# Performance work log

Hardware: AMD Instinct MI355X
Metric: run time of the kernel (lower is better)

Reference implementation:

```python
import jax, jax.numpy as jnp
import numpy as np

NB, L, A, FEAT = 4, 256, 14, 128
MAX_AA, MAX_RELPOS = 22, 32
ATOM_N, ATOM_CA, ATOM_C = 0, 1, 2
INFEAT = 3 * FEAT + 26  # 26 = AngularEncoding.get_out_dim(2)
FREQ = jnp.array([1.0, 2.0, 3.0, 1.0, 0.5, 1.0 / 3.0], jnp.float32)


def _dihedral(p0, p1, p2, p3):
    v0 = p2 - p1
    v1 = p0 - p1
    v2 = p3 - p2
    u1 = jnp.cross(v0, v1)
    u2 = jnp.cross(v0, v2)
    n1 = u1 / jnp.linalg.norm(u1, axis=-1, keepdims=True)
    n2 = u2 / jnp.linalg.norm(u2, axis=-1, keepdims=True)
    sgn = jnp.sign(jnp.sum(jnp.cross(v1, v2) * v0, axis=-1))
    dihed = sgn * jnp.arccos(jnp.clip(jnp.sum(n1 * n2, axis=-1), -0.999999, 0.999999))
    return jnp.nan_to_num(dihed)


def _pairwise_dihedrals(pos_atoms):
    pN = pos_atoms[:, :, ATOM_N]
    pCA = pos_atoms[:, :, ATOM_CA]
    pC = pos_atoms[:, :, ATOM_C]
    ir_phi = _dihedral(pC[:, :, None], pN[:, None, :], pCA[:, None, :], pC[:, None, :])
    ir_psi = _dihedral(pN[:, :, None], pCA[:, :, None], pC[:, :, None], pN[:, None, :])
    return jnp.stack([ir_phi, ir_psi], axis=-1)  # (N, L, L, 2)


def _angular_encode(x):
    # x: (..., 2) -> (..., 26): per-angle [x, sin(x*f_k), cos(x*f_k)] with 6 freq bands
    xe = x[..., None]
    code = jnp.concatenate([xe, jnp.sin(xe * FREQ), jnp.cos(xe * FREQ)], axis=-1)  # (..., 2, 13)
    return code.reshape(x.shape[:-1] + (-1,))


def _forward(aa, res_nb, chain_nb, pos_atoms, mask_atoms,
             aa_pair_embed, relpos_embed, distcoef_embed,
             dist_w1, dist_b1, dist_w2, dist_b2,
             out_w1, out_b1, out_w2, out_b2, out_w3, out_b3):
    N, Ln = aa.shape
    mask_res = mask_atoms[:, :, ATOM_CA]                      # (N, L)
    mask_pair = mask_res[:, :, None] * mask_res[:, None, :]   # (N, L, L)
    aa_pair = aa[:, :, None] * MAX_AA + aa[:, None, :]        # (N, L, L)
    feat_aapair = aa_pair_embed[aa_pair]                      # (N, L, L, F)
    same_chain = chain_nb[:, :, None] == chain_nb[:, None, :]
    relpos = jnp.clip(res_nb[:, :, None] - res_nb[:, None, :], -MAX_RELPOS, MAX_RELPOS)
    feat_relpos = relpos_embed[relpos + MAX_RELPOS] * same_chain[..., None]
    # pairwise atom distances: (N, L, L, A, A) -> (N, L, L, A*A), angstrom -> nm
    diff = pos_atoms[:, :, None, :, None, :] - pos_atoms[:, None, :, None, :, :]
    d = (jnp.linalg.norm(diff, axis=-1) / 10.0).reshape(N, Ln, Ln, A * A)
    c = jax.nn.softplus(distcoef_embed[aa_pair])              # (N, L, L, A*A)
    d_gauss = jnp.exp(-c * d * d)
    mask_ap = (mask_atoms[:, :, None, :, None] * mask_atoms[:, None, :, None, :]).reshape(N, Ln, Ln, A * A)
    h = jax.nn.relu((d_gauss * mask_ap) @ dist_w1 + dist_b1)
    feat_dist = jax.nn.relu(h @ dist_w2 + dist_b2)
    feat_dihed = _angular_encode(_pairwise_dihedrals(pos_atoms))
    feat_all = jnp.concatenate([feat_aapair, feat_relpos, feat_dist, feat_dihed], axis=-1)
    h = jax.nn.relu(feat_all @ out_w1 + out_b1)
    h = jax.nn.relu(h @ out_w2 + out_b2)
    out = h @ out_w3 + out_b3
    return out * mask_pair[..., None]


def setup_inputs() -> dict:
    key = jax.random.key(0)
    ks = jax.random.split(key, 14)
    inp = {}
    inp['aa'] = jax.random.randint(ks[0], (NB, L), 0, MAX_AA)
    inp['res_nb'] = jnp.sort(jax.random.randint(ks[1], (NB, L), 0, 400), axis=-1)
    inp['chain_nb'] = jax.random.randint(ks[2], (NB, L), 0, 2)
    inp['pos_atoms'] = jax.random.normal(ks[3], (NB, L, A, 3), jnp.float32) * 3.0
    inp['mask_atoms'] = jnp.ones((NB, L, A), jnp.float32)
    inp['aa_pair_embed'] = jax.random.normal(ks[4], (MAX_AA * MAX_AA, FEAT), jnp.float32) * 0.02
    inp['relpos_embed'] = jax.random.normal(ks[5], (2 * MAX_RELPOS + 1, FEAT), jnp.float32) * 0.02
    inp['distcoef_embed'] = jax.random.normal(ks[6], (MAX_AA * MAX_AA, A * A), jnp.float32) * 0.01
    inp['dist_w1'] = jax.random.normal(ks[7], (A * A, FEAT), jnp.float32) * 0.05
    inp['dist_b1'] = jnp.zeros((FEAT,), jnp.float32)
    inp['dist_w2'] = jax.random.normal(ks[8], (FEAT, FEAT), jnp.float32) * 0.05
    inp['dist_b2'] = jnp.zeros((FEAT,), jnp.float32)
    inp['out_w1'] = jax.random.normal(ks[9], (INFEAT, FEAT), jnp.float32) * 0.05
    inp['out_b1'] = jnp.zeros((FEAT,), jnp.float32)
    inp['out_w2'] = jax.random.normal(ks[10], (FEAT, FEAT), jnp.float32) * 0.05
    inp['out_b2'] = jnp.zeros((FEAT,), jnp.float32)
    inp['out_w3'] = jax.random.normal(ks[11], (FEAT, FEAT), jnp.float32) * 0.05
    inp['out_b3'] = jnp.zeros((FEAT,), jnp.float32)
    return inp


def reference(aa, res_nb, chain_nb, pos_atoms, mask_atoms,
              aa_pair_embed, relpos_embed, distcoef_embed,
              dist_w1, dist_b1, dist_w2, dist_b2,
              out_w1, out_b1, out_w2, out_b2, out_w3, out_b3):
    return _forward(aa, res_nb, chain_nb, pos_atoms, mask_atoms,
                    aa_pair_embed, relpos_embed, distcoef_embed,
                    dist_w1, dist_b1, dist_w2, dist_b2,
                    out_w1, out_b1, out_w2, out_b2, out_w3, out_b3)
```

## Files before the change

### kernel.cpp

```cpp
#include <hip/hip_runtime.h>
#include <math.h>

typedef unsigned short u16;
typedef __attribute__((ext_vector_type(4))) float f32x4;
typedef __attribute__((ext_vector_type(8))) __bf16 bf16x8;

#define NBATCH 4
#define LL 256
#define AT 14
#define ABD 196
#define NAA 484
#define NREL 65

#define WS_SP   0
#define WS_TAA  94864
#define WS_TREL 156816
#define WS_BF   165136
#define UW1_OFF 0
#define UW2_OFF 32768
#define UW3_OFF 49152
#define UW4_OFF 69632
#define UW5_OFF 86016

__device__ __forceinline__ u16 f2bf(float f) {
    unsigned u = __builtin_bit_cast(unsigned, f);
    u += 0x7fffu + ((u >> 16) & 1u);
    return (u16)(u >> 16);
}

struct F3 { float x, y, z; };
__device__ __forceinline__ F3 f3sub(F3 a, F3 b){ return {a.x-b.x, a.y-b.y, a.z-b.z}; }
__device__ __forceinline__ F3 f3cross(F3 a, F3 b){
    return {a.y*b.z - a.z*b.y, a.z*b.x - a.x*b.z, a.x*b.y - a.y*b.x};
}
__device__ __forceinline__ float f3dot(F3 a, F3 b){ return a.x*b.x + a.y*b.y + a.z*b.z; }

__device__ __forceinline__ float dihedral_f(F3 p0, F3 p1, F3 p2, F3 p3) {
    F3 v0 = f3sub(p2, p1);
    F3 v1 = f3sub(p0, p1);
    F3 v2 = f3sub(p3, p2);
    F3 u1 = f3cross(v0, v1);
    F3 u2 = f3cross(v0, v2);
    float q1 = f3dot(u1, u1), q2 = f3dot(u2, u2);
    float co = f3dot(u1, u2) / sqrtf(q1 * q2);
    co = fminf(fmaxf(co, -0.999999f), 0.999999f);
    float s = f3dot(f3cross(v1, v2), v0);
    float sg = (s > 0.f) ? 1.f : ((s < 0.f) ? -1.f : 0.f);
    float d = sg * acosf(co);
    if (q1 == 0.f || q2 == 0.f || !isfinite(d)) d = 0.f;
    return d;
}


__global__ void prep_sp(const float* __restrict__ dc, float* __restrict__ ws) {
    int idx = blockIdx.x * 256 + threadIdx.x;
    if (idx < NAA * ABD) {
        float v = dc[idx];
        ws[WS_SP + idx] = (v > 20.f) ? v : log1pf(expf(v));
    }
}

__global__ void prep_tab(const float* __restrict__ aa_emb, const float* __restrict__ rel_emb,
                         const float* __restrict__ w1, const float* __restrict__ b1,
                         float* __restrict__ ws) {
    int r = blockIdx.x;
    int t = threadIdx.x;
    if (r < NAA) {
        float acc = b1[t];
        for (int k = 0; k < 128; k++) acc += aa_emb[r*128 + k] * w1[k*128 + t];
        ws[WS_TAA + r*128 + t] = acc;
    } else {
        int rr = r - NAA;
        float acc = 0.f;
        for (int k = 0; k < 128; k++) acc += rel_emb[rr*128 + k] * w1[(128 + k)*128 + t];
        ws[WS_TREL + rr*128 + t] = acc;
    }
}

__global__ void prep_wt(const float* __restrict__ dw1, const float* __restrict__ dw2,
                        const float* __restrict__ ow1, const float* __restrict__ ow2,
                        const float* __restrict__ ow3, float* __restrict__ ws) {
    u16* U = (u16*)(ws + WS_BF);
    int idx = blockIdx.x * 256 + threadIdx.x;
    float v; int dst;
    if (idx < 32768) {
        int c = idx >> 8, k = idx & 255;
        v = (k < ABD) ? dw1[k*128 + c] : 0.f;
        dst = UW1_OFF + idx;
    } else if (idx < 49152) {
        int j = idx - 32768; int c = j >> 7, k = j & 127;
        v = dw2[k*128 + c];
        dst = UW2_OFF + j;
    } else if (idx < 69632) {
        int j = idx - 49152; int c = j / 160, k = j - 160*c;
        v = (k < 128) ? ow1[(256 + k)*128 + c]
                      : ((k < 154) ? ow1[(384 + k - 128)*128 + c] : 0.f);
        dst = UW3_OFF + j;
    } else if (idx < 86016) {
        int j = idx - 69632; int c = j >> 7, k = j & 127;
        v = ow2[k*128 + c];
        dst = UW4_OFF + j;
    } else if (idx < 102400) {
        int j = idx - 86016; int c = j >> 7, k = j & 127;
        v = ow3[k*128 + c];
        dst = UW5_OFF + j;
    } else return;
    U[dst] = f2bf(v);
}


template<int NS>
__device__ __forceinline__ void gemm_steps(const char* Al, int rowlog, int swzm,
                                           const u16* __restrict__ Bt, int kstride,
                                           int c0, int l15, int kg,
                                           int kbA, int kbB, f32x4 acc[4][2]) {
#pragma unroll
    for (int s = 0; s < NS; s++) {
        const int koffA = 2*(kbA + s*32 + kg*8);
        bf16x8 a0, a1, a2, a3;
        {
            int row = l15;
            a0 = *(const bf16x8*)(Al + (row << rowlog) + (koffA ^ ((row & swzm) << 4)));
            row = 16 + l15;
            a1 = *(const bf16x8*)(Al + (row << rowlog) + (koffA ^ ((row & swzm) << 4)));
            row = 32 + l15;
            a2 = *(const bf16x8*)(Al + (row << rowlog) + (koffA ^ ((row & swzm) << 4)));
            row = 48 + l15;
            a3 = *(const bf16x8*)(Al + (row << rowlog) + (koffA ^ ((row & swzm) << 4)));
        }
        const u16* bp = Bt + (size_t)(c0 + l15) * kstride + (kbB + s*32 + kg*8);
        bf16x8 b0 = *(const bf16x8*)(bp);
        bf16x8 b1 = *(const bf16x8*)(bp + 16*kstride);
        acc[0][0] = __builtin_amdgcn_mfma_f32_16x16x32_bf16(a0, b0, acc[0][0], 0,0,0);
        acc[0][1] = __builtin_amdgcn_mfma_f32_16x16x32_bf16(a0, b1, acc[0][1], 0,0,0);
        acc[1][0] = __builtin_amdgcn_mfma_f32_16x16x32_bf16(a1, b0, acc[1][0], 0,0,0);
        acc[1][1] = __builtin_amdgcn_mfma_f32_16x16x32_bf16(a1, b1, acc[1][1], 0,0,0);
        acc[2][0] = __builtin_amdgcn_mfma_f32_16x16x32_bf16(a2, b0, acc[2][0], 0,0,0);
        acc[2][1] = __builtin_amdgcn_mfma_f32_16x16x32_bf16(a2, b1, acc[2][1], 0,0,0);
        acc[3][0] = __builtin_amdgcn_mfma_f32_16x16x32_bf16(a3, b0, acc[3][0], 0,0,0);
        acc[3][1] = __builtin_amdgcn_mfma_f32_16x16x32_bf16(a3, b1, acc[3][1], 0,0,0);
    }
}

#define ZACC do { _Pragma("unroll") for (int _r=0;_r<4;_r++) { \
    acc[_r][0] = f32x4{0.f,0.f,0.f,0.f}; acc[_r][1] = f32x4{0.f,0.f,0.f,0.f}; } } while(0)

__launch_bounds__(256, 2)
__global__ void pair_main(const int* __restrict__ aa, const int* __restrict__ res_nb,
                          const int* __restrict__ chain_nb,
                          const float* __restrict__ pos, const float* __restrict__ maskA,
                          const float* __restrict__ dist_b1, const float* __restrict__ dist_b2,
                          const float* __restrict__ out_b2, const float* __restrict__ out_b3,
                          const float* __restrict__ ws, float* __restrict__ out) {
    __shared__ __align__(16) u16 buf_g[64*256];
    __shared__ __align__(16) u16 bufA[64*128];
    __shared__ __align__(16) u16 bufB[64*128];
    __shared__ __align__(16) u16 sdih[64*32];
    __shared__ float sposi[42];
    __shared__ float smaski[14];
    __shared__ int   saap[64];
    __shared__ int   srel[64];
    __shared__ float smjca[64];

    const float* SP   = ws + WS_SP;
    const float* TAA  = ws + WS_TAA;
    const float* TREL = ws + WS_TREL;
    const u16*   UW   = (const u16*)(ws + WS_BF);

    const int t  = threadIdx.x;
    const int bt = blockIdx.x;
    const int jt = bt & 3, i = (bt >> 2) & 255, n = bt >> 10;
    const int j0 = jt * 64;

    const int lane = t & 63, w = t >> 6;
    const int l15 = lane & 15, lg = lane >> 4;
    const int c0w = w * 32;

    float db1c[2], db2c[2], ob2c[2], ob3c[2];
#pragma unroll
    for (int cb = 0; cb < 2; cb++) {
        int col = c0w + cb*16 + l15;
        db1c[cb] = dist_b1[col];
        db2c[cb] = dist_b2[col];
        ob2c[cb] = out_b2[col];
        ob3c[cb] = out_b3[col];
    }

    float* posjf  = (float*)bufA;
    float* maskjf = (float*)bufB;

    const float* posNI  = pos   + (size_t)((n*LL + i)*AT)*3;
    const float* maskNI = maskA + (size_t)(n*LL + i)*AT;
    if (t < 42) sposi[t] = posNI[t];
    if (t >= 64 && t < 78) smaski[t - 64] = maskNI[t - 64];
    const int aa_i = aa[n*LL + i], res_i = res_nb[n*LL + i], ch_i = chain_nb[n*LL + i];
    if (t < 64) {
        int j = j0 + t;
        saap[t] = aa_i*22 + aa[n*LL + j];
        int rp = res_i - res_nb[n*LL + j];
        rp = min(32, max(-32, rp));
        srel[t] = (ch_i == chain_nb[n*LL + j]) ? (rp + 32) : -1;
    }
    for (int e = t; e < 64*AT; e += 256) {
        int j = e / AT, b = e - j*AT;
        int gj = j0 + j;
        maskjf[j*16 + b] = maskA[(size_t)(n*LL + gj)*AT + b];
        const float* ps = pos + (size_t)((n*LL + gj)*AT + b)*3;
        posjf[j*48 + b*3 + 0] = ps[0];
        posjf[j*48 + b*3 + 1] = ps[1];
        posjf[j*48 + b*3 + 2] = ps[2];
    }
    __syncthreads();

    if (t < 64) smjca[t] = maskjf[t*16 + 1];
    if (t < 64) {
        char* sd = (char*)sdih + t*64;
#pragma unroll
        for (int c = 26; c < 32; c++) *(u16*)(sd + ((2*c) ^ ((t & 3) << 4))) = 0;
    }
    if (t < 128) {
        int r = t >> 1, angv = t & 1;
        const float* Pj = posjf + r*48;
        F3 p0, p1, p2, p3;
        if (angv == 0) {
            p0 = {sposi[6], sposi[7], sposi[8]};
            p1 = {Pj[0], Pj[1], Pj[2]};
            p2 = {Pj[3], Pj[4], Pj[5]};
            p3 = {Pj[6], Pj[7], Pj[8]};
        } else {
            p0 = {sposi[0], sposi[1], sposi[2]};
            p1 = {sposi[3], sposi[4], sposi[5]};
            p2 = {sposi[6], sposi[7], sposi[8]};
            p3 = {Pj[0], Pj[1], Pj[2]};
        }
        float dh = dihedral_f(p0, p1, p2, p3);
        const float F[6] = {1.f, 2.f, 3.f, 1.f, 0.5f, 1.f/3.f};
        char* sd = (char*)sdih + r*64;
        int cb0 = angv * 13;
        *(u16*)(sd + ((2*cb0) ^ ((r & 3) << 4))) = f2bf(dh);
#pragma unroll
        for (int q = 0; q < 6; q++) {
            *(u16*)(sd + ((2*(cb0+1+q)) ^ ((r & 3) << 4))) = f2bf(sinf(dh * F[q]));
            *(u16*)(sd + ((2*(cb0+7+q)) ^ ((r & 3) << 4))) = f2bf(cosf(dh * F[q]));
        }
    }
    for (int q = t; q < 3584; q += 256) {
        int r = q / 56, kq = (q - r*56) * 4;
        int sa = saap[r];
        ushort4 pk;
#pragma unroll
        for (int u = 0; u < 4; u++) {
            int k = kq + u;
            float g = 0.f;
            if (k < ABD) {
                int a_ = k / 14, b_ = k - a_*14;
                float dx = sposi[a_*3+0] - posjf[r*48 + b_*3+0];
                float dy = sposi[a_*3+1] - posjf[r*48 + b_*3+1];
                float dz = sposi[a_*3+2] - posjf[r*48 + b_*3+2];
                float d2 = (dx*dx + dy*dy + dz*dz) * 0.01f;
                float c = SP[sa*ABD + k];
                g = __expf(-c * d2) * smaski[a_] * maskjf[r*16 + b_];
            }
            ((u16*)&pk)[u] = f2bf(g);
        }
        *(ushort4*)((char*)buf_g + r*512 + ((2*kq) ^ ((r & 7) << 4))) = pk;
    }
    __syncthreads();

    f32x4 acc[4][2];

    ZACC;
    gemm_steps<7>((const char*)buf_g, 9, 7, UW + UW1_OFF, 256, c0w, l15, lg, 0, 0, acc);
#pragma unroll
    for (int rb = 0; rb < 4; rb++)
#pragma unroll
        for (int cb = 0; cb < 2; cb++)
#pragma unroll
            for (int rg = 0; rg < 4; rg++) {
                int row = rb*16 + lg*4 + rg;
                int col = c0w + cb*16 + l15;
                float v = fmaxf(acc[rb][cb][rg] + db1c[cb], 0.f);
                *(u16*)((char*)bufA + row*256 + ((2*col) ^ ((row & 7) << 4))) = f2bf(v);
            }
    __syncthreads();

    ZACC;
    for (int q = t; q < 2048; q += 256) {
        int r = q >> 5, c4 = (q & 31) * 4;
        float4 v = *(const float4*)(TAA + saap[r]*128 + c4);
        if (srel[r] >= 0) {
            float4 u2 = *(const float4*)(TREL + srel[r]*128 + c4);
            v.x += u2.x; v.y += u2.y; v.z += u2.z; v.w += u2.w;
        }
        *(float4*)((char*)buf_g + r*512 + ((4*c4) ^ ((r & 7) << 4))) = v;
    }
    gemm_steps<4>((const char*)bufA, 8, 7, UW + UW2_OFF, 128, c0w, l15, lg, 0, 0, acc);
#pragma unroll
    for (int rb = 0; rb < 4; rb++)
#pragma unroll
        for (int cb = 0; cb < 2; cb++)
#pragma unroll
            for (int rg = 0; rg < 4; rg++) {
                int row = rb*16 + lg*4 + rg;
                int col = c0w + cb*16 + l15;
                float v = fmaxf(acc[rb][cb][rg] + db2c[cb], 0.f);
                *(u16*)((char*)bufB + row*256 + ((2*col) ^ ((row & 7) << 4))) = f2bf(v);
            }
    __syncthreads();

    ZACC;
    gemm_steps<4>((const char*)bufB, 8, 7, UW + UW3_OFF, 160, c0w, l15, lg, 0, 0, acc);
    gemm_steps<1>((const char*)sdih, 6, 3, UW + UW3_OFF, 160, c0w, l15, lg, 0, 128, acc);
#pragma unroll
    for (int rb = 0; rb < 4; rb++)
#pragma unroll
        for (int cb = 0; cb < 2; cb++)
#pragma unroll
            for (int rg = 0; rg < 4; rg++) {
                int row = rb*16 + lg*4 + rg;
                int col = c0w + cb*16 + l15;
                float ts = *(const float*)((char*)buf_g + row*512 + ((4*col) ^ ((row & 7) << 4)));
                float v = fmaxf(acc[rb][cb][rg] + ts, 0.f);
                *(u16*)((char*)bufA + row*256 + ((2*col) ^ ((row & 7) << 4))) = f2bf(v);
            }
    __syncthreads();

    ZACC;
    gemm_steps<4>((const char*)bufA, 8, 7, UW + UW4_OFF, 128, c0w, l15, lg, 0, 0, acc);
#pragma unroll
    for (int rb = 0; rb < 4; rb++)
#pragma unroll
        for (int cb = 0; cb < 2; cb++)
#pragma unroll
            for (int rg = 0; rg < 4; rg++) {
                int row = rb*16 + lg*4 + rg;
                int col = c0w + cb*16 + l15;
                float v = fmaxf(acc[rb][cb][rg] + ob2c[cb], 0.f);
                *(u16*)((char*)bufB + row*256 + ((2*col) ^ ((row & 7) << 4))) = f2bf(v);
            }
    __syncthreads();

    ZACC;
    gemm_steps<4>((const char*)bufB, 8, 7, UW + UW5_OFF, 128, c0w, l15, lg, 0, 0, acc);
    {
        float mi = smaski[1];
#pragma unroll
        for (int rb = 0; rb < 4; rb++)
#pragma unroll
            for (int cb = 0; cb < 2; cb++)
#pragma unroll
                for (int rg = 0; rg < 4; rg++) {
                    int row = rb*16 + lg*4 + rg;
                    int col = c0w + cb*16 + l15;
                    float mp = mi * smjca[row];
                    out[((size_t)(n*LL + i)*LL + j0 + row)*128 + col] =
                        (acc[rb][cb][rg] + ob3c[cb]) * mp;
                }
    }
}


extern "C" void kernel_launch(void* const* d_in, const int* in_sizes, int n_in,
                              void* d_out, int out_size, void* d_ws, size_t ws_size,
                              hipStream_t stream) {
    const int*   aa       = (const int*)d_in[0];
    const int*   res_nb   = (const int*)d_in[1];
    const int*   chain_nb = (const int*)d_in[2];
    const float* pos      = (const float*)d_in[3];
    const float* maskA    = (const float*)d_in[4];
    const float* aa_emb   = (const float*)d_in[5];
    const float* rel_emb  = (const float*)d_in[6];
    const float* distcoef = (const float*)d_in[7];
    const float* dw1      = (const float*)d_in[8];
    const float* db1      = (const float*)d_in[9];
    const float* dw2      = (const float*)d_in[10];
    const float* db2      = (const float*)d_in[11];
    const float* ow1      = (const float*)d_in[12];
    const float* ob1      = (const float*)d_in[13];
    const float* ow2      = (const float*)d_in[14];
    const float* ob2      = (const float*)d_in[15];
    const float* ow3      = (const float*)d_in[16];
    const float* ob3      = (const float*)d_in[17];
    float* ws  = (float*)d_ws;
    float* out = (float*)d_out;

    prep_sp<<<(NAA*ABD + 255)/256, 256, 0, stream>>>(distcoef, ws);
    prep_tab<<<NAA + NREL, 128, 0, stream>>>(aa_emb, rel_emb, ow1, ob1, ws);
    prep_wt<<<400, 256, 0, stream>>>(dw1, dw2, ow1, ow2, ow3, ws);
    pair_main<<<NBATCH*LL*4, 256, 0, stream>>>(aa, res_nb, chain_nb, pos, maskA,
                                               db1, db2, ob2, ob3, ws, out);
}
```

Measured before the change: 391.6 us.

## Transpose MFMA operands so weights are the A operand and output tiles vectorize

Swaps the MFMA operand roles: weight rows now supply the A fragment from global memory and activations in shared memory supply B. Each lane's accumulator then holds four consecutive output columns, so epilogues write packed ushort4 to LDS and float4 to the output. The triple-buffer LDS layout becomes two buffers, and the TAA/TREL table values are read straight from global in the third epilogue instead of being staged in LDS. Occupancy is raised to 3 blocks per CU, which risks register pressure and spills.

```diff
diff --git a/kernel.cpp b/kernel.cpp
--- a/kernel.cpp
+++ b/kernel.cpp
@@ -10,17 +10,16 @@
 #define AT 14
 #define ABD 196
 #define NAA 484
-#define NREL 65
 
 #define WS_SP   0
 #define WS_TAA  94864
 #define WS_TREL 156816
 #define WS_BF   165136
-#define UW1_OFF 0
-#define UW2_OFF 32768
-#define UW3_OFF 49152
-#define UW4_OFF 69632
-#define UW5_OFF 86016
+#define UW1 0
+#define UW2 32768
+#define UW3 49152
+#define UW4 69632
+#define UW5 86016
 
 __device__ __forceinline__ u16 f2bf(float f) {
     unsigned u = __builtin_bit_cast(unsigned, f);
@@ -86,81 +85,86 @@
     if (idx < 32768) {
         int c = idx >> 8, k = idx & 255;
         v = (k < ABD) ? dw1[k*128 + c] : 0.f;
-        dst = UW1_OFF + idx;
+        dst = UW1 + idx;
     } else if (idx < 49152) {
         int j = idx - 32768; int c = j >> 7, k = j & 127;
         v = dw2[k*128 + c];
-        dst = UW2_OFF + j;
+        dst = UW2 + j;
     } else if (idx < 69632) {
         int j = idx - 49152; int c = j / 160, k = j - 160*c;
         v = (k < 128) ? ow1[(256 + k)*128 + c]
                       : ((k < 154) ? ow1[(384 + k - 128)*128 + c] : 0.f);
-        dst = UW3_OFF + j;
+        dst = UW3 + j;
     } else if (idx < 86016) {
         int j = idx - 69632; int c = j >> 7, k = j & 127;
         v = ow2[k*128 + c];
-        dst = UW4_OFF + j;
+        dst = UW4 + j;
     } else if (idx < 102400) {
         int j = idx - 86016; int c = j >> 7, k = j & 127;
         v = ow3[k*128 + c];
-        dst = UW5_OFF + j;
+        dst = UW5 + j;
     } else return;
     U[dst] = f2bf(v);
 }
 
 
-template<int NS>
-__device__ __forceinline__ void gemm_steps(const char* Al, int rowlog, int swzm,
-                                           const u16* __restrict__ Bt, int kstride,
-                                           int c0, int l15, int kg,
-                                           int kbA, int kbB, f32x4 acc[4][2]) {
+template<int NS, int RLOG>
+__device__ __forceinline__ void gemmO(const u16* Sact, const u16* __restrict__ Wt, int kst,
+                                      int kbA, int kbB, const int* r16, int bswz, int lg,
+                                      int wl15, f32x4 acc[2][4]) {
+    const u16* aP0 = Wt + (size_t)wl15 * kst + kbA + lg*8;
+    const u16* aP1 = aP0 + (size_t)16 * kst;
+    const char* Sb = (const char*)Sact;
 #pragma unroll
     for (int s = 0; s < NS; s++) {
-        const int koffA = 2*(kbA + s*32 + kg*8);
-        bf16x8 a0, a1, a2, a3;
-        {
-            int row = l15;
-            a0 = *(const bf16x8*)(Al + (row << rowlog) + (koffA ^ ((row & swzm) << 4)));
-            row = 16 + l15;
-            a1 = *(const bf16x8*)(Al + (row << rowlog) + (koffA ^ ((row & swzm) << 4)));
-            row = 32 + l15;
-            a2 = *(const bf16x8*)(Al + (row << rowlog) + (koffA ^ ((row & swzm) << 4)));
-            row = 48 + l15;
-            a3 = *(const bf16x8*)(Al + (row << rowlog) + (koffA ^ ((row & swzm) << 4)));
-        }
-        const u16* bp = Bt + (size_t)(c0 + l15) * kstride + (kbB + s*32 + kg*8);
-        bf16x8 b0 = *(const bf16x8*)(bp);
-        bf16x8 b1 = *(const bf16x8*)(bp + 16*kstride);
-        acc[0][0] = __builtin_amdgcn_mfma_f32_16x16x32_bf16(a0, b0, acc[0][0], 0,0,0);
-        acc[0][1] = __builtin_amdgcn_mfma_f32_16x16x32_bf16(a0, b1, acc[0][1], 0,0,0);
-        acc[1][0] = __builtin_amdgcn_mfma_f32_16x16x32_bf16(a1, b0, acc[1][0], 0,0,0);
-        acc[1][1] = __builtin_amdgcn_mfma_f32_16x16x32_bf16(a1, b1, acc[1][1], 0,0,0);
-        acc[2][0] = __builtin_amdgcn_mfma_f32_16x16x32_bf16(a2, b0, acc[2][0], 0,0,0);
-        acc[2][1] = __builtin_amdgcn_mfma_f32_16x16x32_bf16(a2, b1, acc[2][1], 0,0,0);
-        acc[3][0] = __builtin_amdgcn_mfma_f32_16x16x32_bf16(a3, b0, acc[3][0], 0,0,0);
-        acc[3][1] = __builtin_amdgcn_mfma_f32_16x16x32_bf16(a3, b1, acc[3][1], 0,0,0);
-    }
-}
-
-#define ZACC do { _Pragma("unroll") for (int _r=0;_r<4;_r++) { \
-    acc[_r][0] = f32x4{0.f,0.f,0.f,0.f}; acc[_r][1] = f32x4{0.f,0.f,0.f,0.f}; } } while(0)
-
-__launch_bounds__(256, 2)
+        bf16x8 af0 = *(const bf16x8*)(aP0 + s*32);
+        bf16x8 af1 = *(const bf16x8*)(aP1 + s*32);
+        int inrow = (((kbB + s*32)*2) + lg*16) ^ bswz;
+        bf16x8 b0 = *(const bf16x8*)(Sb + (r16[0] << RLOG) + inrow);
+        bf16x8 b1 = *(const bf16x8*)(Sb + (r16[1] << RLOG) + inrow);
+        bf16x8 b2 = *(const bf16x8*)(Sb + (r16[2] << RLOG) + inrow);
+        bf16x8 b3 = *(const bf16x8*)(Sb + (r16[3] << RLOG) + inrow);
+        acc[0][0] = __builtin_amdgcn_mfma_f32_16x16x32_bf16(af0, b0, acc[0][0], 0,0,0);
+        acc[0][1] = __builtin_amdgcn_mfma_f32_16x16x32_bf16(af0, b1, acc[0][1], 0,0,0);
+        acc[0][2] = __builtin_amdgcn_mfma_f32_16x16x32_bf16(af0, b2, acc[0][2], 0,0,0);
+        acc[0][3] = __builtin_amdgcn_mfma_f32_16x16x32_bf16(af0, b3, acc[0][3], 0,0,0);
+        acc[1][0] = __builtin_amdgcn_mfma_f32_16x16x32_bf16(af1, b0, acc[1][0], 0,0,0);
+        acc[1][1] = __builtin_amdgcn_mfma_f32_16x16x32_bf16(af1, b1, acc[1][1], 0,0,0);
+        acc[1][2] = __builtin_amdgcn_mfma_f32_16x16x32_bf16(af1, b2, acc[1][2], 0,0,0);
+        acc[1][3] = __builtin_amdgcn_mfma_f32_16x16x32_bf16(af1, b3, acc[1][3], 0,0,0);
+    }
+}
+
+#define ZACC do { _Pragma("unroll") for (int _m = 0; _m < 2; _m++) \
+    { acc[_m][0] = f32x4{0.f,0.f,0.f,0.f}; acc[_m][1] = f32x4{0.f,0.f,0.f,0.f}; \
+      acc[_m][2] = f32x4{0.f,0.f,0.f,0.f}; acc[_m][3] = f32x4{0.f,0.f,0.f,0.f}; } } while(0)
+
+#define EPI_WRITE(DST, RL, BV) do { \
+  _Pragma("unroll") for (int mt = 0; mt < 2; mt++) { \
+    float4 bb = BV[mt]; int cb2 = (cq0 + mt*16)*2; \
+    _Pragma("unroll") for (int ct = 0; ct < 4; ct++) { \
+      ushort4 pk; \
+      pk.x = f2bf(fmaxf(acc[mt][ct][0] + bb.x, 0.f)); \
+      pk.y = f2bf(fmaxf(acc[mt][ct][1] + bb.y, 0.f)); \
+      pk.z = f2bf(fmaxf(acc[mt][ct][2] + bb.z, 0.f)); \
+      pk.w = f2bf(fmaxf(acc[mt][ct][3] + bb.w, 0.f)); \
+      *(ushort4*)((char*)(DST) + (r16[ct] << (RL)) + (cb2 ^ swz)) = pk; \
+    } } } while(0)
+
+__launch_bounds__(256, 3)
 __global__ void pair_main(const int* __restrict__ aa, const int* __restrict__ res_nb,
                           const int* __restrict__ chain_nb,
                           const float* __restrict__ pos, const float* __restrict__ maskA,
                           const float* __restrict__ dist_b1, const float* __restrict__ dist_b2,
                           const float* __restrict__ out_b2, const float* __restrict__ out_b3,
                           const float* __restrict__ ws, float* __restrict__ out) {
-    __shared__ __align__(16) u16 buf_g[64*256];
-    __shared__ __align__(16) u16 bufA[64*128];
-    __shared__ __align__(16) u16 bufB[64*128];
+    __shared__ __align__(16) u16 SB[64*256];
+    __shared__ __align__(16) u16 SA[64*128];
     __shared__ __align__(16) u16 sdih[64*32];
     __shared__ float sposi[42];
     __shared__ float smaski[14];
     __shared__ int   saap[64];
     __shared__ int   srel[64];
-    __shared__ float smjca[64];
 
     const float* SP   = ws + WS_SP;
     const float* TAA  = ws + WS_TAA;
@@ -174,20 +178,25 @@
 
     const int lane = t & 63, w = t >> 6;
     const int l15 = lane & 15, lg = lane >> 4;
-    const int c0w = w * 32;
-
-    float db1c[2], db2c[2], ob2c[2], ob3c[2];
-#pragma unroll
-    for (int cb = 0; cb < 2; cb++) {
-        int col = c0w + cb*16 + l15;
-        db1c[cb] = dist_b1[col];
-        db2c[cb] = dist_b2[col];
-        ob2c[cb] = out_b2[col];
-        ob3c[cb] = out_b3[col];
-    }
-
-    float* posjf  = (float*)bufA;
-    float* maskjf = (float*)bufB;
+    const int swz = (l15 & 7) << 4;
+    const int wl15 = w*32 + l15;
+    const int cq0 = w*32 + lg*4;
+    int r16[4];
+#pragma unroll
+    for (int ct = 0; ct < 4; ct++) r16[ct] = ct*16 + l15;
+
+    float4 db1v[2], db2v[2], ob2v[2], ob3v[2];
+#pragma unroll
+    for (int mt = 0; mt < 2; mt++) {
+        int cq = cq0 + mt*16;
+        db1v[mt] = *(const float4*)(dist_b1 + cq);
+        db2v[mt] = *(const float4*)(dist_b2 + cq);
+        ob2v[mt] = *(const float4*)(out_b2 + cq);
+        ob3v[mt] = *(const float4*)(out_b3 + cq);
+    }
+
+    float* posjf  = (float*)SA;
+    float* maskjf = (float*)SA + 64*42;
 
     const float* posNI  = pos   + (size_t)((n*LL + i)*AT)*3;
     const float* maskNI = maskA + (size_t)(n*LL + i)*AT;
@@ -204,15 +213,45 @@
     for (int e = t; e < 64*AT; e += 256) {
         int j = e / AT, b = e - j*AT;
         int gj = j0 + j;
-        maskjf[j*16 + b] = maskA[(size_t)(n*LL + gj)*AT + b];
+        maskjf[e] = maskA[(size_t)(n*LL + gj)*AT + b];
         const float* ps = pos + (size_t)((n*LL + gj)*AT + b)*3;
-        posjf[j*48 + b*3 + 0] = ps[0];
-        posjf[j*48 + b*3 + 1] = ps[1];
-        posjf[j*48 + b*3 + 2] = ps[2];
-    }
-    __syncthreads();
-
-    if (t < 64) smjca[t] = maskjf[t*16 + 1];
+        posjf[j*42 + b*3 + 0] = ps[0];
+        posjf[j*42 + b*3 + 1] = ps[1];
+        posjf[j*42 + b*3 + 2] = ps[2];
+    }
+    __syncthreads();
+
+    int saR[4], srR[4]; float mjR[4];
+#pragma unroll
+    for (int ct = 0; ct < 4; ct++) {
+        saR[ct] = saap[r16[ct]];
+        srR[ct] = srel[r16[ct]];
+        mjR[ct] = maskjf[r16[ct]*AT + 1];
+    }
+    const float mi = smaski[1];
+
+    for (int q = t; q < 3584; q += 256) {
+        int r = q / 56, kq = (q - r*56) * 4;
+        int sa = saap[r];
+        ushort4 pk;
+#pragma unroll
+        for (int u = 0; u < 4; u++) {
+            int k = kq + u;
+            float g = 0.f;
+            if (k < ABD) {
+                int a_ = k / 14, b_ = k - a_*14;
+                float dx = sposi[a_*3+0] - posjf[r*42 + b_*3+0];
+                float dy = sposi[a_*3+1] - posjf[r*42 + b_*3+1];
+                float dz = sposi[a_*3+2] - posjf[r*42 + b_*3+2];
+                float d2 = (dx*dx + dy*dy + dz*dz) * 0.01f;
+                float c = SP[sa*ABD + k];
+                g = __expf(-c * d2) * smaski[a_] * maskjf[r*AT + b_];
+            }
+            ((u16*)&pk)[u] = f2bf(g);
+        }
+        *(ushort4*)((char*)SB + r*512 + ((2*kq) ^ ((r & 7) << 4))) = pk;
+    }
+
     if (t < 64) {
         char* sd = (char*)sdih + t*64;
 #pragma unroll
@@ -220,7 +259,7 @@
     }
     if (t < 128) {
         int r = t >> 1, angv = t & 1;
-        const float* Pj = posjf + r*48;
+        const float* Pj = posjf + r*42;
         F3 p0, p1, p2, p3;
         if (angv == 0) {
             p0 = {sposi[6], sposi[7], sposi[8]};
@@ -234,128 +273,75 @@
             p3 = {Pj[0], Pj[1], Pj[2]};
         }
         float dh = dihedral_f(p0, p1, p2, p3);
+        char* sd = (char*)sdih + r*64;
+        int szd = (r & 3) << 4;
+        int cb0 = angv * 13;
         const float F[6] = {1.f, 2.f, 3.f, 1.f, 0.5f, 1.f/3.f};
-        char* sd = (char*)sdih + r*64;
-        int cb0 = angv * 13;
-        *(u16*)(sd + ((2*cb0) ^ ((r & 3) << 4))) = f2bf(dh);
+        *(u16*)(sd + ((2*cb0) ^ szd)) = f2bf(dh);
 #pragma unroll
         for (int q = 0; q < 6; q++) {
-            *(u16*)(sd + ((2*(cb0+1+q)) ^ ((r & 3) << 4))) = f2bf(sinf(dh * F[q]));
-            *(u16*)(sd + ((2*(cb0+7+q)) ^ ((r & 3) << 4))) = f2bf(cosf(dh * F[q]));
-        }
-    }
-    for (int q = t; q < 3584; q += 256) {
-        int r = q / 56, kq = (q - r*56) * 4;
-        int sa = saap[r];
-        ushort4 pk;
-#pragma unroll
-        for (int u = 0; u < 4; u++) {
-            int k = kq + u;
-            float g = 0.f;
-            if (k < ABD) {
-                int a_ = k / 14, b_ = k - a_*14;
-                float dx = sposi[a_*3+0] - posjf[r*48 + b_*3+0];
-                float dy = sposi[a_*3+1] - posjf[r*48 + b_*3+1];
-                float dz = sposi[a_*3+2] - posjf[r*48 + b_*3+2];
-                float d2 = (dx*dx + dy*dy + dz*dz) * 0.01f;
-                float c = SP[sa*ABD + k];
-                g = __expf(-c * d2) * smaski[a_] * maskjf[r*16 + b_];
+            *(u16*)(sd + ((2*(cb0+1+q)) ^ szd)) = f2bf(sinf(dh * F[q]));
+            *(u16*)(sd + ((2*(cb0+7+q)) ^ szd)) = f2bf(cosf(dh * F[q]));
+        }
+    }
+    __syncthreads();
+
+    f32x4 acc[2][4];
+
+    ZACC;
+    gemmO<7,9>((const u16*)SB, UW + UW1, 256, 0, 0, r16, swz, lg, wl15, acc);
+    EPI_WRITE(SA, 8, db1v);
+    __syncthreads();
+
+    ZACC;
+    gemmO<4,8>((const u16*)SA, UW + UW2, 128, 0, 0, r16, swz, lg, wl15, acc);
+    EPI_WRITE(SB, 9, db2v);
+    __syncthreads();
+
+    ZACC;
+    gemmO<4,9>((const u16*)SB, UW + UW3, 160, 0, 0, r16, swz, lg, wl15, acc);
+    gemmO<1,6>(sdih, UW + UW3, 160, 128, 0, r16, (l15 & 3) << 4, lg, wl15, acc);
+#pragma unroll
+    for (int mt = 0; mt < 2; mt++) {
+        int cq = cq0 + mt*16; int cb2 = cq*2;
+#pragma unroll
+        for (int ct = 0; ct < 4; ct++) {
+            float4 tv = *(const float4*)(TAA + (size_t)saR[ct]*128 + cq);
+            if (srR[ct] >= 0) {
+                float4 u2 = *(const float4*)(TREL + (size_t)srR[ct]*128 + cq);
+                tv.x += u2.x; tv.y += u2.y; tv.z += u2.z; tv.w += u2.w;
             }
-            ((u16*)&pk)[u] = f2bf(g);
-        }
-        *(ushort4*)((char*)buf_g + r*512 + ((2*kq) ^ ((r & 7) << 4))) = pk;
-    }
-    __syncthreads();
-
-    f32x4 acc[4][2];
-
-    ZACC;
-    gemm_steps<7>((const char*)buf_g, 9, 7, UW + UW1_OFF, 256, c0w, l15, lg, 0, 0, acc);
-#pragma unroll
-    for (int rb = 0; rb < 4; rb++)
-#pragma unroll
-        for (int cb = 0; cb < 2; cb++)
-#pragma unroll
-            for (int rg = 0; rg < 4; rg++) {
-                int row = rb*16 + lg*4 + rg;
-                int col = c0w + cb*16 + l15;
-                float v = fmaxf(acc[rb][cb][rg] + db1c[cb], 0.f);
-                *(u16*)((char*)bufA + row*256 + ((2*col) ^ ((row & 7) << 4))) = f2bf(v);
-            }
-    __syncthreads();
-
-    ZACC;
-    for (int q = t; q < 2048; q += 256) {
-        int r = q >> 5, c4 = (q & 31) * 4;
-        float4 v = *(const float4*)(TAA + saap[r]*128 + c4);
-        if (srel[r] >= 0) {
-            float4 u2 = *(const float4*)(TREL + srel[r]*128 + c4);
-            v.x += u2.x; v.y += u2.y; v.z += u2.z; v.w += u2.w;
-        }
-        *(float4*)((char*)buf_g + r*512 + ((4*c4) ^ ((r & 7) << 4))) = v;
-    }
-    gemm_steps<4>((const char*)bufA, 8, 7, UW + UW2_OFF, 128, c0w, l15, lg, 0, 0, acc);
-#pragma unroll
-    for (int rb = 0; rb < 4; rb++)
-#pragma unroll
-        for (int cb = 0; cb < 2; cb++)
-#pragma unroll
-            for (int rg = 0; rg < 4; rg++) {
-                int row = rb*16 + lg*4 + rg;
-                int col = c0w + cb*16 + l15;
-                float v = fmaxf(acc[rb][cb][rg] + db2c[cb], 0.f);
-                *(u16*)((char*)bufB + row*256 + ((2*col) ^ ((row & 7) << 4))) = f2bf(v);
-            }
-    __syncthreads();
-
-    ZACC;
-    gemm_steps<4>((const char*)bufB, 8, 7, UW + UW3_OFF, 160, c0w, l15, lg, 0, 0, acc);
-    gemm_steps<1>((const char*)sdih, 6, 3, UW + UW3_OFF, 160, c0w, l15, lg, 0, 128, acc);
-#pragma unroll
-    for (int rb = 0; rb < 4; rb++)
-#pragma unroll
-        for (int cb = 0; cb < 2; cb++)
-#pragma unroll
-            for (int rg = 0; rg < 4; rg++) {
-                int row = rb*16 + lg*4 + rg;
-                int col = c0w + cb*16 + l15;
-                float ts = *(const float*)((char*)buf_g + row*512 + ((4*col) ^ ((row & 7) << 4)));
-                float v = fmaxf(acc[rb][cb][rg] + ts, 0.f);
-                *(u16*)((char*)bufA + row*256 + ((2*col) ^ ((row & 7) << 4))) = f2bf(v);
-            }
-    __syncthreads();
-
-    ZACC;
-    gemm_steps<4>((const char*)bufA, 8, 7, UW + UW4_OFF, 128, c0w, l15, lg, 0, 0, acc);
-#pragma unroll
-    for (int rb = 0; rb < 4; rb++)
-#pragma unroll
-        for (int cb = 0; cb < 2; cb++)
-#pragma unroll
-            for (int rg = 0; rg < 4; rg++) {
-                int row = rb*16 + lg*4 + rg;
-                int col = c0w + cb*16 + l15;
-                float v = fmaxf(acc[rb][cb][rg] + ob2c[cb], 0.f);
-                *(u16*)((char*)bufB + row*256 + ((2*col) ^ ((row & 7) << 4))) = f2bf(v);
-            }
-    __syncthreads();
-
-    ZACC;
-    gemm_steps<4>((const char*)bufB, 8, 7, UW + UW5_OFF, 128, c0w, l15, lg, 0, 0, acc);
-    {
-        float mi = smaski[1];
-#pragma unroll
-        for (int rb = 0; rb < 4; rb++)
-#pragma unroll
-            for (int cb = 0; cb < 2; cb++)
-#pragma unroll
-                for (int rg = 0; rg < 4; rg++) {
-                    int row = rb*16 + lg*4 + rg;
-                    int col = c0w + cb*16 + l15;
-                    float mp = mi * smjca[row];
-                    out[((size_t)(n*LL + i)*LL + j0 + row)*128 + col] =
-                        (acc[rb][cb][rg] + ob3c[cb]) * mp;
-                }
+            ushort4 pk;
+            pk.x = f2bf(fmaxf(acc[mt][ct][0] + tv.x, 0.f));
+            pk.y = f2bf(fmaxf(acc[mt][ct][1] + tv.y, 0.f));
+            pk.z = f2bf(fmaxf(acc[mt][ct][2] + tv.z, 0.f));
+            pk.w = f2bf(fmaxf(acc[mt][ct][3] + tv.w, 0.f));
+            *(ushort4*)((char*)SA + (r16[ct] << 8) + (cb2 ^ swz)) = pk;
+        }
+    }
+    __syncthreads();
+
+    ZACC;
+    gemmO<4,8>((const u16*)SA, UW + UW4, 128, 0, 0, r16, swz, lg, wl15, acc);
+    EPI_WRITE(SB, 9, ob2v);
+    __syncthreads();
+
+    ZACC;
+    gemmO<4,9>((const u16*)SB, UW + UW5, 128, 0, 0, r16, swz, lg, wl15, acc);
+#pragma unroll
+    for (int mt = 0; mt < 2; mt++) {
+        int cq = cq0 + mt*16;
+        float4 bb = ob3v[mt];
+#pragma unroll
+        for (int ct = 0; ct < 4; ct++) {
+            float mp = mi * mjR[ct];
+            float4 v;
+            v.x = (acc[mt][ct][0] + bb.x) * mp;
+            v.y = (acc[mt][ct][1] + bb.y) * mp;
+            v.z = (acc[mt][ct][2] + bb.z) * mp;
+            v.w = (acc[mt][ct][3] + bb.w) * mp;
+            *(float4*)(out + ((size_t)((n*LL + i)*LL) + j0 + r16[ct]) * 128 + cq) = v;
+        }
     }
 }
 
@@ -385,7 +371,7 @@
     float* out = (float*)d_out;
 
     prep_sp<<<(NAA*ABD + 255)/256, 256, 0, stream>>>(distcoef, ws);
-    prep_tab<<<NAA + NREL, 128, 0, stream>>>(aa_emb, rel_emb, ow1, ob1, ws);
+    prep_tab<<<NAA + 65, 128, 0, stream>>>(aa_emb, rel_emb, ow1, ob1, ws);
     prep_wt<<<400, 256, 0, stream>>>(dw1, dw2, ow1, ow2, ow3, ws);
     pair_main<<<NBATCH*LL*4, 256, 0, stream>>>(aa, res_nb, chain_nb, pos, maskA,
                                                db1, db2, ob2, ob3, ws, out);
```

Result: no change. 385.9 us (-1.4%).
